# Performance work log

Hardware: AMD Instinct MI355X
Metric: run time of the kernel (lower is better)

Reference implementation:

```python
import jax, jax.numpy as jnp
import numpy as np

N_NODES = 100000
N_EDGES = 600000
HIDDEN = 128
ALPHA = 0.1
K_HOPS = 10


def setup_inputs() -> dict:
    key = jax.random.key(0)
    k1, k2, k3, k4 = jax.random.split(key, 4)
    x = jax.random.normal(k1, (N_NODES, HIDDEN), dtype=jnp.float32)
    edge_index = jax.random.randint(k2, (2, N_EDGES), 0, N_NODES, dtype=jnp.int64)
    W = jax.random.normal(k3, (HIDDEN, HIDDEN), dtype=jnp.float32) * (1.0 / np.sqrt(HIDDEN))
    b = jax.random.normal(k4, (HIDDEN,), dtype=jnp.float32) * 0.01
    return {"x": x, "edge_index": edge_index, "W": W, "b": b}


def reference(x, edge_index, W, b):
    N = x.shape[0]
    # Linear projection (PyTorch convention: y = x W^T + b)
    h = x @ W.T + b

    # gcn_norm with added self-loops (PyG APPNPConv default)
    loop = jnp.arange(N, dtype=edge_index.dtype)
    src = jnp.concatenate([edge_index[0], loop])  # [E+N]
    dst = jnp.concatenate([edge_index[1], loop])
    ones = jnp.ones(src.shape[0], dtype=h.dtype)
    deg = jax.ops.segment_sum(ones, dst, num_segments=N)  # in-degree incl. self-loop
    dinv = jnp.where(deg > 0, jax.lax.rsqrt(deg), 0.0)
    norm = dinv[src] * dinv[dst]  # [E+N]

    # APPNP propagation: h <- (1-alpha) * A_hat h + alpha * h0
    h0 = h
    for _ in range(K_HOPS):
        msg = norm[:, None] * h[src]  # gather + scale
        agg = jax.ops.segment_sum(msg, dst, num_segments=N)  # scatter-add
        h = (1.0 - ALPHA) * agg + ALPHA * h0
    return h
```

## Files before the change

### kernel.cpp

```cpp
#include <hip/hip_runtime.h>

#define N_NODES_C 100000
#define N_EDGES_C 600000
#define HIDDEN_C 128
#define K_HOPS_C 10
#define SCAN_B 98

typedef short short8 __attribute__((ext_vector_type(8)));
typedef float f32x16 __attribute__((ext_vector_type(16)));

__device__ __forceinline__ unsigned short f2bf(float f) {
    unsigned u = __float_as_uint(f);
    return (unsigned short)((u + 0x7FFFu + ((u >> 16) & 1u)) >> 16);
}
__device__ __forceinline__ float bf_lo(unsigned p) { return __uint_as_float(p << 16); }
__device__ __forceinline__ float bf_hi(unsigned p) { return __uint_as_float(p & 0xFFFF0000u); }

__global__ void k_deg(const int* __restrict__ dst, int* __restrict__ deg,
                      unsigned short* __restrict__ rank, int E) {
    int e = blockIdx.x * blockDim.x + threadIdx.x;
    if (e < E) {
        int r = atomicAdd(&deg[dst[e]], 1);
        rank[e] = (unsigned short)r;
    }
}

__global__ __launch_bounds__(1024) void k_scan_a(const int* __restrict__ deg,
                                                 int* __restrict__ offs,
                                                 int* __restrict__ blksum,
                                                 float* __restrict__ dinv,
                                                 int* __restrict__ deghist, int N) {
    __shared__ int wtot[16];
    __shared__ int lhist[64];
    int tid = threadIdx.x;
    int i = blockIdx.x * 1024 + tid;
    int lane = tid & 63;
    int wid = tid >> 6;
    if (tid < 64) lhist[tid] = 0;
    __syncthreads();
    int v = (i < N) ? deg[i] : 0;
    if (i < N) {
        dinv[i] = rsqrtf((float)(v + 1));
        atomicAdd(&lhist[v < 63 ? v : 63], 1);
    }
    int incl = v;
#pragma unroll
    for (int d = 1; d < 64; d <<= 1) {
        int t = __shfl_up(incl, (unsigned)d, 64);
        if (lane >= d) incl += t;
    }
    if (lane == 63) wtot[wid] = incl;
    __syncthreads();
    int woff = 0, btot = 0;
#pragma unroll
    for (int w = 0; w < 16; ++w) {
        int t = wtot[w];
        if (w < wid) woff += t;
        btot += t;
    }
    if (i < N) offs[i] = woff + incl - v;
    if (tid == 0) blksum[blockIdx.x] = btot;
    if (tid < 64 && lhist[tid] != 0) atomicAdd(&deghist[tid], lhist[tid]);
}

__global__ __launch_bounds__(128) void k_scan_b(const int* __restrict__ blksum,
                                                int* __restrict__ blkoff,
                                                int* __restrict__ offs,
                                                const int* __restrict__ deghist,
                                                int* __restrict__ bucketcur,
                                                int NB, int N) {
    __shared__ int wt[2];
    int t = threadIdx.x;
    int lane = t & 63;
    int w = t >> 6;
    int v = (t < NB) ? blksum[t] : 0;
    int incl = v;
#pragma unroll
    for (int d = 1; d < 64; d <<= 1) {
        int s = __shfl_up(incl, (unsigned)d, 64);
        if (lane >= d) incl += s;
    }
    if (lane == 63) wt[w] = incl;
    __syncthreads();
    int excl = incl - v + (w == 1 ? wt[0] : 0);
    if (t < NB) blkoff[t] = excl;
    if (t == 127) offs[N] = wt[0] + wt[1];
    if (w == 0) {
        int hv = deghist[lane];
        int hincl = hv;
#pragma unroll
        for (int d = 1; d < 64; d <<= 1) {
            int s = __shfl_up(hincl, (unsigned)d, 64);
            if (lane >= d) hincl += s;
        }
        bucketcur[lane] = hincl - hv;
    }
}

__global__ __launch_bounds__(1024) void k_scan_c(int* __restrict__ offs,
                                                 const int* __restrict__ blkoff,
                                                 const int* __restrict__ deg,
                                                 const float* __restrict__ dinv,
                                                 int* __restrict__ bucketcur,
                                                 uint4* __restrict__ meta,
                                                 int* __restrict__ inv, int N) {
    __shared__ int lcnt[64];
    __shared__ int lbase[64];
    int tid = threadIdx.x;
    int i = blockIdx.x * 1024 + tid;
    if (tid < 64) lcnt[tid] = 0;
    __syncthreads();
    int v = 0, d = 0, b = 0, lpos = 0;
    if (i < N) {
        v = offs[i] + blkoff[blockIdx.x];
        offs[i] = v;
        d = deg[i];
        b = d < 63 ? d : 63;
        lpos = atomicAdd(&lcnt[b], 1);
    }
    __syncthreads();
    if (tid < 64) lbase[tid] = (lcnt[tid] != 0) ? atomicAdd(&bucketcur[tid], lcnt[tid]) : 0;
    __syncthreads();
    if (i < N) {
        int pos = lbase[b] + lpos;
        float dv = dinv[i];
        meta[pos] = make_uint4((unsigned)v, (unsigned)(v + d), (unsigned)i,
                               __float_as_uint(dv * dv));
        inv[i] = pos;
    }
}

__global__ void k_fill(const int* __restrict__ src, const int* __restrict__ dst,
                       const unsigned short* __restrict__ rank,
                       const float* __restrict__ dinv, const int* __restrict__ offs,
                       const int* __restrict__ inv,
                       uint2* __restrict__ csr, int E) {
    int e = blockIdx.x * blockDim.x + threadIdx.x;
    if (e < E) {
        int s = src[e], d = dst[e];
        int pos = offs[d] + (int)rank[e];
        uint2 v;
        v.x = (unsigned)inv[s];
        v.y = __float_as_uint(dinv[s] * dinv[d]);
        csr[pos] = v;
    }
}

__global__ __launch_bounds__(256) void k_gemm(const float* __restrict__ x,
                                              const float* __restrict__ W,
                                              const float* __restrict__ b,
                                              const int* __restrict__ inv,
                                              unsigned short* __restrict__ hb, int N) {
    __shared__ unsigned short Wb[HIDDEN_C * HIDDEN_C];
    int tid = threadIdx.x;
#pragma unroll
    for (int i = 0; i < 8; ++i) {
        int c = tid + 256 * i;
        int m = c >> 4;
        int g = c & 15;
        const float4* wsrc = (const float4*)W + m * 32 + g * 2;
        float4 wa = wsrc[0];
        float4 wb = wsrc[1];
        unsigned short t8[8];
        t8[0] = f2bf(wa.x); t8[1] = f2bf(wa.y); t8[2] = f2bf(wa.z); t8[3] = f2bf(wa.w);
        t8[4] = f2bf(wb.x); t8[5] = f2bf(wb.y); t8[6] = f2bf(wb.z); t8[7] = f2bf(wb.w);
        int gs = g ^ (m & 15);
        *(uint4*)&Wb[m * 128 + gs * 8] = *(const uint4*)t8;
    }
    __syncthreads();

    int lane = tid & 63;
    int wv = tid >> 6;
    int row0 = blockIdx.x * 128 + wv * 32;
    int m = lane & 31;
    int half = lane >> 5;

    int row = row0 + m;
    if (row >= N) row = N - 1;
    const float4* xrow = (const float4*)(x + (size_t)row * 128);

    f32x16 acc[4];
#pragma unroll
    for (int t = 0; t < 4; ++t)
#pragma unroll
        for (int r = 0; r < 16; ++r) acc[t][r] = 0.f;

    for (int s = 0; s < 8; ++s) {
        int kb = s * 16 + half * 8;
        float4 x0 = xrow[kb >> 2];
        float4 x1 = xrow[(kb >> 2) + 1];
        union { unsigned short u[8]; short8 v; } af;
        af.u[0] = f2bf(x0.x); af.u[1] = f2bf(x0.y); af.u[2] = f2bf(x0.z); af.u[3] = f2bf(x0.w);
        af.u[4] = f2bf(x1.x); af.u[5] = f2bf(x1.y); af.u[6] = f2bf(x1.z); af.u[7] = f2bf(x1.w);
        int g = kb >> 3;
#pragma unroll
        for (int t = 0; t < 4; ++t) {
            int r = t * 32 + m;
            short8 bfrag = *(const short8*)&Wb[r * 128 + ((g ^ (r & 15)) << 3)];
            acc[t] = __builtin_amdgcn_mfma_f32_32x32x16_bf16(af.v, bfrag, acc[t], 0, 0, 0);
        }
    }

    float bias[4];
#pragma unroll
    for (int t = 0; t < 4; ++t) bias[t] = b[t * 32 + m];
#pragma unroll
    for (int t = 0; t < 4; ++t) {
#pragma unroll
        for (int r = 0; r < 16; ++r) {
            int rrow = (r & 3) + 8 * (r >> 2) + 4 * half;
            int node = row0 + rrow;
            if (node < N) {
                int slot = inv[node];
                float v = acc[t][r] + bias[t];
                hb[(size_t)slot * 128 + t * 32 + m] = f2bf(v);
            }
        }
    }
}

__global__ __launch_bounds__(256) void k_prop(const uint4* __restrict__ hin4,
                                              const uint4* __restrict__ h04,
                                              uint4* __restrict__ hout_b,
                                              float* __restrict__ hout_f,
                                              const uint4* __restrict__ meta,
                                              const uint2* __restrict__ csr,
                                              int N, int final_hop) {
    int tid = threadIdx.x;
    int lane = tid & 63;
    int wid = tid >> 6;
    int q = lane >> 4;
    int f = lane & 15;

    int slot = (blockIdx.x * 4 + wid) * 4 + q;
    bool valid = slot < N;

    int node = 0, beg = 0, end = 0;
    float ws = 0.f;
    if (valid) {
        uint4 m = meta[slot];
        beg = (int)m.x;
        end = (int)m.y;
        node = (int)m.z;
        ws = __uint_as_float(m.w);
    }

    uint4 hq = make_uint4(0u, 0u, 0u, 0u);
    uint4 ps = make_uint4(0u, 0u, 0u, 0u);
    if (valid) {
        hq = h04[(size_t)slot * 16 + f];
        ps = hin4[(size_t)slot * 16 + f];
    }

    float acc[8];
#pragma unroll
    for (int i = 0; i < 8; ++i) acc[i] = 0.f;

#pragma unroll 2
    for (int j = beg; j < end; j += 4) {
        int j1 = (j + 1 < end) ? j + 1 : j;
        int j2 = (j + 2 < end) ? j + 2 : j;
        int j3 = (j + 3 < end) ? j + 3 : j;
        uint2 e0 = csr[j];
        uint2 e1 = csr[j1];
        uint2 e2 = csr[j2];
        uint2 e3 = csr[j3];
        uint4 p0 = hin4[(size_t)e0.x * 16 + f];
        uint4 p1 = hin4[(size_t)e1.x * 16 + f];
        uint4 p2 = hin4[(size_t)e2.x * 16 + f];
        uint4 p3 = hin4[(size_t)e3.x * 16 + f];
        float w0 = __uint_as_float(e0.y);
        float w1 = (j + 1 < end) ? __uint_as_float(e1.y) : 0.f;
        float w2 = (j + 2 < end) ? __uint_as_float(e2.y) : 0.f;
        float w3 = (j + 3 < end) ? __uint_as_float(e3.y) : 0.f;
        acc[0] += w0 * bf_lo(p0.x); acc[1] += w0 * bf_hi(p0.x);
        acc[2] += w0 * bf_lo(p0.y); acc[3] += w0 * bf_hi(p0.y);
        acc[4] += w0 * bf_lo(p0.z); acc[5] += w0 * bf_hi(p0.z);
        acc[6] += w0 * bf_lo(p0.w); acc[7] += w0 * bf_hi(p0.w);
        acc[0] += w1 * bf_lo(p1.x); acc[1] += w1 * bf_hi(p1.x);
        acc[2] += w1 * bf_lo(p1.y); acc[3] += w1 * bf_hi(p1.y);
        acc[4] += w1 * bf_lo(p1.z); acc[5] += w1 * bf_hi(p1.z);
        acc[6] += w1 * bf_lo(p1.w); acc[7] += w1 * bf_hi(p1.w);
        acc[0] += w2 * bf_lo(p2.x); acc[1] += w2 * bf_hi(p2.x);
        acc[2] += w2 * bf_lo(p2.y); acc[3] += w2 * bf_hi(p2.y);
        acc[4] += w2 * bf_lo(p2.z); acc[5] += w2 * bf_hi(p2.z);
        acc[6] += w2 * bf_lo(p2.w); acc[7] += w2 * bf_hi(p2.w);
        acc[0] += w3 * bf_lo(p3.x); acc[1] += w3 * bf_hi(p3.x);
        acc[2] += w3 * bf_lo(p3.y); acc[3] += w3 * bf_hi(p3.y);
        acc[4] += w3 * bf_lo(p3.z); acc[5] += w3 * bf_hi(p3.z);
        acc[6] += w3 * bf_lo(p3.w); acc[7] += w3 * bf_hi(p3.w);
    }

    acc[0] += ws * bf_lo(ps.x); acc[1] += ws * bf_hi(ps.x);
    acc[2] += ws * bf_lo(ps.y); acc[3] += ws * bf_hi(ps.y);
    acc[4] += ws * bf_lo(ps.z); acc[5] += ws * bf_hi(ps.z);
    acc[6] += ws * bf_lo(ps.w); acc[7] += ws * bf_hi(ps.w);

    if (valid) {
        float o[8];
        o[0] = 0.9f * acc[0] + 0.1f * bf_lo(hq.x);
        o[1] = 0.9f * acc[1] + 0.1f * bf_hi(hq.x);
        o[2] = 0.9f * acc[2] + 0.1f * bf_lo(hq.y);
        o[3] = 0.9f * acc[3] + 0.1f * bf_hi(hq.y);
        o[4] = 0.9f * acc[4] + 0.1f * bf_lo(hq.z);
        o[5] = 0.9f * acc[5] + 0.1f * bf_hi(hq.z);
        o[6] = 0.9f * acc[6] + 0.1f * bf_lo(hq.w);
        o[7] = 0.9f * acc[7] + 0.1f * bf_hi(hq.w);
        if (final_hop) {
            float4* dst0 = (float4*)(hout_f + (size_t)node * 128 + f * 8);
            float4 v0; v0.x = o[0]; v0.y = o[1]; v0.z = o[2]; v0.w = o[3];
            float4 v1; v1.x = o[4]; v1.y = o[5]; v1.z = o[6]; v1.w = o[7];
            dst0[0] = v0;
            dst0[1] = v1;
        } else {
            uint4 p;
            p.x = (unsigned)f2bf(o[0]) | ((unsigned)f2bf(o[1]) << 16);
            p.y = (unsigned)f2bf(o[2]) | ((unsigned)f2bf(o[3]) << 16);
            p.z = (unsigned)f2bf(o[4]) | ((unsigned)f2bf(o[5]) << 16);
            p.w = (unsigned)f2bf(o[6]) | ((unsigned)f2bf(o[7]) << 16);
            hout_b[(size_t)slot * 16 + f] = p;
        }
    }
}

extern "C" void kernel_launch(void* const* d_in, const int* in_sizes, int n_in,
                              void* d_out, int out_size, void* d_ws, size_t ws_size,
                              hipStream_t stream) {
    const float* x = (const float*)d_in[0];
    const int* edge = (const int*)d_in[1];
    const float* W = (const float*)d_in[2];
    const float* b = (const float*)d_in[3];
    float* out = (float*)d_out;

    const int N = N_NODES_C;
    const int E = N_EDGES_C;
    const int* src = edge;
    const int* dst = edge + E;

    char* ws = (char*)d_ws;
    size_t off = 0;
    auto carve = [&](size_t bytes) -> void* {
        void* p = ws + off;
        off = (off + bytes + 511) & ~(size_t)511;
        return p;
    };
    unsigned short* h0b = (unsigned short*)carve((size_t)N * HIDDEN_C * 2);
    unsigned short* bA  = (unsigned short*)carve((size_t)N * HIDDEN_C * 2);
    unsigned short* bB  = (unsigned short*)carve((size_t)N * HIDDEN_C * 2);
    int*   deg     = (int*)  carve(((size_t)N + 64) * sizeof(int));
    int*   deghist = deg + N;
    float* dinv    = (float*)carve((size_t)N * sizeof(float));
    int*   offs    = (int*)  carve((size_t)(N + 1) * sizeof(int));
    unsigned short* rank = (unsigned short*)carve((size_t)E * sizeof(unsigned short));
    uint2* csr     = (uint2*)carve((size_t)E * sizeof(uint2));
    int*   blksum  = (int*)  carve((size_t)SCAN_B * sizeof(int));
    int*   blkoff  = (int*)  carve((size_t)SCAN_B * sizeof(int));
    int*   bucketcur = (int*)carve(64 * sizeof(int));
    uint4* meta    = (uint4*)carve((size_t)N * sizeof(uint4));
    int*   inv     = (int*)  carve((size_t)N * sizeof(int));
    (void)ws_size;

    hipMemsetAsync(deg, 0, ((size_t)N + 64) * sizeof(int), stream);

    int eb = (E + 255) / 256;
    k_deg<<<eb, 256, 0, stream>>>(dst, deg, rank, E);
    k_scan_a<<<SCAN_B, 1024, 0, stream>>>(deg, offs, blksum, dinv, deghist, N);
    k_scan_b<<<1, 128, 0, stream>>>(blksum, blkoff, offs, deghist, bucketcur, SCAN_B, N);
    k_scan_c<<<SCAN_B, 1024, 0, stream>>>(offs, blkoff, deg, dinv, bucketcur, meta, inv, N);
    k_fill<<<eb, 256, 0, stream>>>(src, dst, rank, dinv, offs, inv, csr, E);

    k_gemm<<<(N + 127) / 128, 256, 0, stream>>>(x, W, b, inv, h0b, N);

    const uint4* hin = (const uint4*)h0b;
    for (int k = 0; k < K_HOPS_C; ++k) {
        int fin = (k == K_HOPS_C - 1);
        uint4* houtb = ((k & 1) == 0) ? (uint4*)bA : (uint4*)bB;
        k_prop<<<(N + 15) / 16, 256, 0, stream>>>(hin, (const uint4*)h0b,
                                                  fin ? nullptr : houtb,
                                                  fin ? out : nullptr,
                                                  meta, csr, N, fin);
        hin = houtb;
    }
}
```

Measured before the change: 506.8 us.

## Fuse ten propagation hops into one persistent kernel with grid barriers

Replaces the ten per-hop k_prop launches with a single persistent kernel of 1024 blocks. Waves grid-stride over node quads and synchronize between hops with an atomic-counter grid barrier. This removes per-launch overhead and the tail gaps between hops. It also walks quads in reverse order, apparently so the heaviest-degree slots go first. The risks are barrier spin cost, lower parallelism than the original roughly 6250 blocks, and deadlock if all 1024 blocks cannot be co-resident.

Result: slower. 1.776 ms (+250.4%).

```diff
diff --git a/kernel.cpp b/kernel.cpp
--- a/kernel.cpp
+++ b/kernel.cpp
@@ -5,6 +5,7 @@
 #define HIDDEN_C 128
 #define K_HOPS_C 10
 #define SCAN_B 98
+#define PROP_BLOCKS 1024
 
 typedef short short8 __attribute__((ext_vector_type(8)));
 typedef float f32x16 __attribute__((ext_vector_type(16)));
@@ -219,107 +220,142 @@
     }
 }
 
-__global__ __launch_bounds__(256) void k_prop(const uint4* __restrict__ hin4,
-                                              const uint4* __restrict__ h04,
-                                              uint4* __restrict__ hout_b,
-                                              float* __restrict__ hout_f,
-                                              const uint4* __restrict__ meta,
-                                              const uint2* __restrict__ csr,
-                                              int N, int final_hop) {
+__device__ __forceinline__ void grid_barrier(int* bar, int nblocks, int gen) {
+    __syncthreads();
+    if (threadIdx.x == 0) {
+        int prev = __hip_atomic_fetch_add(&bar[0], 1, __ATOMIC_ACQ_REL,
+                                          __HIP_MEMORY_SCOPE_AGENT);
+        if (prev == nblocks - 1) {
+            __hip_atomic_store(&bar[0], 0, __ATOMIC_RELAXED, __HIP_MEMORY_SCOPE_AGENT);
+            __hip_atomic_store(&bar[1], gen + 1, __ATOMIC_RELEASE,
+                               __HIP_MEMORY_SCOPE_AGENT);
+        } else {
+            while (__hip_atomic_load(&bar[1], __ATOMIC_ACQUIRE,
+                                     __HIP_MEMORY_SCOPE_AGENT) <= gen) {
+                __builtin_amdgcn_s_sleep(2);
+            }
+        }
+    }
+    __syncthreads();
+}
+
+__global__ __launch_bounds__(256, 4) void k_prop10(const uint4* __restrict__ h04,
+                                                   uint4* __restrict__ bufA,
+                                                   uint4* __restrict__ bufB,
+                                                   float* __restrict__ hout_f,
+                                                   const uint4* __restrict__ meta,
+                                                   const uint2* __restrict__ csr,
+                                                   int* __restrict__ bar,
+                                                   int N) {
     int tid = threadIdx.x;
     int lane = tid & 63;
     int wid = tid >> 6;
     int q = lane >> 4;
     int f = lane & 15;
 
-    int slot = (blockIdx.x * 4 + wid) * 4 + q;
-    bool valid = slot < N;
-
-    int node = 0, beg = 0, end = 0;
-    float ws = 0.f;
-    if (valid) {
-        uint4 m = meta[slot];
-        beg = (int)m.x;
-        end = (int)m.y;
-        node = (int)m.z;
-        ws = __uint_as_float(m.w);
-    }
-
-    uint4 hq = make_uint4(0u, 0u, 0u, 0u);
-    uint4 ps = make_uint4(0u, 0u, 0u, 0u);
-    if (valid) {
-        hq = h04[(size_t)slot * 16 + f];
-        ps = hin4[(size_t)slot * 16 + f];
-    }
-
-    float acc[8];
-#pragma unroll
-    for (int i = 0; i < 8; ++i) acc[i] = 0.f;
+    int nquads = (N + 3) >> 2;
+    int wave_g = blockIdx.x * 4 + wid;
+    int nwaves = gridDim.x * 4;
+
+    for (int k = 0; k < K_HOPS_C; ++k) {
+        const uint4* hin4 = (k == 0) ? h04 : ((k & 1) ? bufA : bufB);
+        uint4* houtb = (k & 1) ? bufB : bufA;
+        int fin = (k == K_HOPS_C - 1);
+
+        for (int t = wave_g; t < nquads; t += nwaves) {
+            int quad = nquads - 1 - t;
+            int slot = quad * 4 + q;
+            bool valid = slot < N;
+
+            int node = 0, beg = 0, end = 0;
+            float ws = 0.f;
+            if (valid) {
+                uint4 m = meta[slot];
+                beg = (int)m.x;
+                end = (int)m.y;
+                node = (int)m.z;
+                ws = __uint_as_float(m.w);
+            }
+
+            uint4 hq = make_uint4(0u, 0u, 0u, 0u);
+            uint4 ps = make_uint4(0u, 0u, 0u, 0u);
+            if (valid) {
+                hq = h04[(size_t)slot * 16 + f];
+                ps = hin4[(size_t)slot * 16 + f];
+            }
+
+            float acc[8];
+#pragma unroll
+            for (int i = 0; i < 8; ++i) acc[i] = 0.f;
 
 #pragma unroll 2
-    for (int j = beg; j < end; j += 4) {
-        int j1 = (j + 1 < end) ? j + 1 : j;
-        int j2 = (j + 2 < end) ? j + 2 : j;
-        int j3 = (j + 3 < end) ? j + 3 : j;
-        uint2 e0 = csr[j];
-        uint2 e1 = csr[j1];
-        uint2 e2 = csr[j2];
-        uint2 e3 = csr[j3];
-        uint4 p0 = hin4[(size_t)e0.x * 16 + f];
-        uint4 p1 = hin4[(size_t)e1.x * 16 + f];
-        uint4 p2 = hin4[(size_t)e2.x * 16 + f];
-        uint4 p3 = hin4[(size_t)e3.x * 16 + f];
-        float w0 = __uint_as_float(e0.y);
-        float w1 = (j + 1 < end) ? __uint_as_float(e1.y) : 0.f;
-        float w2 = (j + 2 < end) ? __uint_as_float(e2.y) : 0.f;
-        float w3 = (j + 3 < end) ? __uint_as_float(e3.y) : 0.f;
-        acc[0] += w0 * bf_lo(p0.x); acc[1] += w0 * bf_hi(p0.x);
-        acc[2] += w0 * bf_lo(p0.y); acc[3] += w0 * bf_hi(p0.y);
-        acc[4] += w0 * bf_lo(p0.z); acc[5] += w0 * bf_hi(p0.z);
-        acc[6] += w0 * bf_lo(p0.w); acc[7] += w0 * bf_hi(p0.w);
-        acc[0] += w1 * bf_lo(p1.x); acc[1] += w1 * bf_hi(p1.x);
-        acc[2] += w1 * bf_lo(p1.y); acc[3] += w1 * bf_hi(p1.y);
-        acc[4] += w1 * bf_lo(p1.z); acc[5] += w1 * bf_hi(p1.z);
-        acc[6] += w1 * bf_lo(p1.w); acc[7] += w1 * bf_hi(p1.w);
-        acc[0] += w2 * bf_lo(p2.x); acc[1] += w2 * bf_hi(p2.x);
-        acc[2] += w2 * bf_lo(p2.y); acc[3] += w2 * bf_hi(p2.y);
-        acc[4] += w2 * bf_lo(p2.z); acc[5] += w2 * bf_hi(p2.z);
-        acc[6] += w2 * bf_lo(p2.w); acc[7] += w2 * bf_hi(p2.w);
-        acc[0] += w3 * bf_lo(p3.x); acc[1] += w3 * bf_hi(p3.x);
-        acc[2] += w3 * bf_lo(p3.y); acc[3] += w3 * bf_hi(p3.y);
-        acc[4] += w3 * bf_lo(p3.z); acc[5] += w3 * bf_hi(p3.z);
-        acc[6] += w3 * bf_lo(p3.w); acc[7] += w3 * bf_hi(p3.w);
-    }
-
-    acc[0] += ws * bf_lo(ps.x); acc[1] += ws * bf_hi(ps.x);
-    acc[2] += ws * bf_lo(ps.y); acc[3] += ws * bf_hi(ps.y);
-    acc[4] += ws * bf_lo(ps.z); acc[5] += ws * bf_hi(ps.z);
-    acc[6] += ws * bf_lo(ps.w); acc[7] += ws * bf_hi(ps.w);
-
-    if (valid) {
-        float o[8];
-        o[0] = 0.9f * acc[0] + 0.1f * bf_lo(hq.x);
-        o[1] = 0.9f * acc[1] + 0.1f * bf_hi(hq.x);
-        o[2] = 0.9f * acc[2] + 0.1f * bf_lo(hq.y);
-        o[3] = 0.9f * acc[3] + 0.1f * bf_hi(hq.y);
-        o[4] = 0.9f * acc[4] + 0.1f * bf_lo(hq.z);
-        o[5] = 0.9f * acc[5] + 0.1f * bf_hi(hq.z);
-        o[6] = 0.9f * acc[6] + 0.1f * bf_lo(hq.w);
-        o[7] = 0.9f * acc[7] + 0.1f * bf_hi(hq.w);
-        if (final_hop) {
-            float4* dst0 = (float4*)(hout_f + (size_t)node * 128 + f * 8);
-            float4 v0; v0.x = o[0]; v0.y = o[1]; v0.z = o[2]; v0.w = o[3];
-            float4 v1; v1.x = o[4]; v1.y = o[5]; v1.z = o[6]; v1.w = o[7];
-            dst0[0] = v0;
-            dst0[1] = v1;
-        } else {
-            uint4 p;
-            p.x = (unsigned)f2bf(o[0]) | ((unsigned)f2bf(o[1]) << 16);
-            p.y = (unsigned)f2bf(o[2]) | ((unsigned)f2bf(o[3]) << 16);
-            p.z = (unsigned)f2bf(o[4]) | ((unsigned)f2bf(o[5]) << 16);
-            p.w = (unsigned)f2bf(o[6]) | ((unsigned)f2bf(o[7]) << 16);
-            hout_b[(size_t)slot * 16 + f] = p;
+            for (int j = beg; j < end; j += 4) {
+                int j1 = (j + 1 < end) ? j + 1 : j;
+                int j2 = (j + 2 < end) ? j + 2 : j;
+                int j3 = (j + 3 < end) ? j + 3 : j;
+                uint2 e0 = csr[j];
+                uint2 e1 = csr[j1];
+                uint2 e2 = csr[j2];
+                uint2 e3 = csr[j3];
+                uint4 p0 = hin4[(size_t)e0.x * 16 + f];
+                uint4 p1 = hin4[(size_t)e1.x * 16 + f];
+                uint4 p2 = hin4[(size_t)e2.x * 16 + f];
+                uint4 p3 = hin4[(size_t)e3.x * 16 + f];
+                float w0 = __uint_as_float(e0.y);
+                float w1 = (j + 1 < end) ? __uint_as_float(e1.y) : 0.f;
+                float w2 = (j + 2 < end) ? __uint_as_float(e2.y) : 0.f;
+                float w3 = (j + 3 < end) ? __uint_as_float(e3.y) : 0.f;
+                acc[0] += w0 * bf_lo(p0.x); acc[1] += w0 * bf_hi(p0.x);
+                acc[2] += w0 * bf_lo(p0.y); acc[3] += w0 * bf_hi(p0.y);
+                acc[4] += w0 * bf_lo(p0.z); acc[5] += w0 * bf_hi(p0.z);
+                acc[6] += w0 * bf_lo(p0.w); acc[7] += w0 * bf_hi(p0.w);
+                acc[0] += w1 * bf_lo(p1.x); acc[1] += w1 * bf_hi(p1.x);
+                acc[2] += w1 * bf_lo(p1.y); acc[3] += w1 * bf_hi(p1.y);
+                acc[4] += w1 * bf_lo(p1.z); acc[5] += w1 * bf_hi(p1.z);
+                acc[6] += w1 * bf_lo(p1.w); acc[7] += w1 * bf_hi(p1.w);
+                acc[0] += w2 * bf_lo(p2.x); acc[1] += w2 * bf_hi(p2.x);
+                acc[2] += w2 * bf_lo(p2.y); acc[3] += w2 * bf_hi(p2.y);
+                acc[4] += w2 * bf_lo(p2.z); acc[5] += w2 * bf_hi(p2.z);
+                acc[6] += w2 * bf_lo(p2.w); acc[7] += w2 * bf_hi(p2.w);
+                acc[0] += w3 * bf_lo(p3.x); acc[1] += w3 * bf_hi(p3.x);
+                acc[2] += w3 * bf_lo(p3.y); acc[3] += w3 * bf_hi(p3.y);
+                acc[4] += w3 * bf_lo(p3.z); acc[5] += w3 * bf_hi(p3.z);
+                acc[6] += w3 * bf_lo(p3.w); acc[7] += w3 * bf_hi(p3.w);
+            }
+
+            acc[0] += ws * bf_lo(ps.x); acc[1] += ws * bf_hi(ps.x);
+            acc[2] += ws * bf_lo(ps.y); acc[3] += ws * bf_hi(ps.y);
+            acc[4] += ws * bf_lo(ps.z); acc[5] += ws * bf_hi(ps.z);
+            acc[6] += ws * bf_lo(ps.w); acc[7] += ws * bf_hi(ps.w);
+
+            if (valid) {
+                float o[8];
+                o[0] = 0.9f * acc[0] + 0.1f * bf_lo(hq.x);
+                o[1] = 0.9f * acc[1] + 0.1f * bf_hi(hq.x);
+                o[2] = 0.9f * acc[2] + 0.1f * bf_lo(hq.y);
+                o[3] = 0.9f * acc[3] + 0.1f * bf_hi(hq.y);
+                o[4] = 0.9f * acc[4] + 0.1f * bf_lo(hq.z);
+                o[5] = 0.9f * acc[5] + 0.1f * bf_hi(hq.z);
+                o[6] = 0.9f * acc[6] + 0.1f * bf_lo(hq.w);
+                o[7] = 0.9f * acc[7] + 0.1f * bf_hi(hq.w);
+                if (fin) {
+                    float4* dst0 = (float4*)(hout_f + (size_t)node * 128 + f * 8);
+                    float4 v0; v0.x = o[0]; v0.y = o[1]; v0.z = o[2]; v0.w = o[3];
+                    float4 v1; v1.x = o[4]; v1.y = o[5]; v1.z = o[6]; v1.w = o[7];
+                    dst0[0] = v0;
+                    dst0[1] = v1;
+                } else {
+                    uint4 p;
+                    p.x = (unsigned)f2bf(o[0]) | ((unsigned)f2bf(o[1]) << 16);
+                    p.y = (unsigned)f2bf(o[2]) | ((unsigned)f2bf(o[3]) << 16);
+                    p.z = (unsigned)f2bf(o[4]) | ((unsigned)f2bf(o[5]) << 16);
+                    p.w = (unsigned)f2bf(o[6]) | ((unsigned)f2bf(o[7]) << 16);
+                    houtb[(size_t)slot * 16 + f] = p;
+                }
+            }
         }
+
+        if (!fin) grid_barrier(bar, gridDim.x, k);
     }
 }
 
@@ -347,8 +383,9 @@
     unsigned short* h0b = (unsigned short*)carve((size_t)N * HIDDEN_C * 2);
     unsigned short* bA  = (unsigned short*)carve((size_t)N * HIDDEN_C * 2);
     unsigned short* bB  = (unsigned short*)carve((size_t)N * HIDDEN_C * 2);
-    int*   deg     = (int*)  carve(((size_t)N + 64) * sizeof(int));
+    int*   deg     = (int*)  carve(((size_t)N + 80) * sizeof(int));
     int*   deghist = deg + N;
+    int*   bar     = deg + N + 64;
     float* dinv    = (float*)carve((size_t)N * sizeof(float));
     int*   offs    = (int*)  carve((size_t)(N + 1) * sizeof(int));
     unsigned short* rank = (unsigned short*)carve((size_t)E * sizeof(unsigned short));
@@ -360,7 +397,7 @@
     int*   inv     = (int*)  carve((size_t)N * sizeof(int));
     (void)ws_size;
 
-    hipMemsetAsync(deg, 0, ((size_t)N + 64) * sizeof(int), stream);
+    hipMemsetAsync(deg, 0, ((size_t)N + 80) * sizeof(int), stream);
 
     int eb = (E + 255) / 256;
     k_deg<<<eb, 256, 0, stream>>>(dst, deg, rank, E);
@@ -371,14 +408,6 @@
 
     k_gemm<<<(N + 127) / 128, 256, 0, stream>>>(x, W, b, inv, h0b, N);
 
-    const uint4* hin = (const uint4*)h0b;
-    for (int k = 0; k < K_HOPS_C; ++k) {
-        int fin = (k == K_HOPS_C - 1);
-        uint4* houtb = ((k & 1) == 0) ? (uint4*)bA : (uint4*)bB;
-        k_prop<<<(N + 15) / 16, 256, 0, stream>>>(hin, (const uint4*)h0b,
-                                                  fin ? nullptr : houtb,
-                                                  fin ? out : nullptr,
-                                                  meta, csr, N, fin);
-        hin = houtb;
-    }
-}
+    k_prop10<<<PROP_BLOCKS, 256, 0, stream>>>((const uint4*)h0b, (uint4*)bA,
+                                              (uint4*)bB, out, meta, csr, bar, N);
+}
```
